# Kernel optimization log

Hardware: AMD Instinct MI355X
Metric: run time of the kernel (lower is better)

## Reference

```python
import jax, jax.numpy as jnp
from jax import lax
import numpy as np

B, L, IN_DIM = 1, 2048, 1024
D_MODEL, D_INNER, D_STATE, DT_RANK, D_CONV, N_LAYERS = 512, 1024, 16, 32, 4, 2


def _ln(x, w, b):
    m = jnp.mean(x, -1, keepdims=True)
    v = jnp.var(x, -1, keepdims=True)
    return (x - m) * lax.rsqrt(v + 1e-5) * w + b


def _rms(x, w):
    return x * lax.rsqrt(jnp.mean(x * x, -1, keepdims=True) + 1e-5) * w


def _assoc_scan(dA, dBx):
    # first-order linear recurrence h_t = dA_t * h_{t-1} + dBx_t via associative scan
    def comb(e1, e2):
        a1, b1 = e1
        a2, b2 = e2
        return a1 * a2, a2 * b1 + b2
    return lax.associative_scan(comb, (dA, dBx), axis=1)[1]


def _mamba_layer(h, in_w, cw, cb, xw, dtw, dtb, alog, Dp, ow, rw):
    hn = _rms(h, rw)                              # pre-norm (RMSNorm)
    xz = hn @ in_w                                # [b,l,2*d_inner]
    xi, z = jnp.split(xz, 2, -1)
    # causal depthwise conv1d (kernel d_conv, left pad d_conv-1)
    xc = lax.conv_general_dilated(xi.transpose(0, 2, 1), cw, (1,), [(D_CONV - 1, 0)],
                                  feature_group_count=D_INNER,
                                  dimension_numbers=('NCH', 'OIH', 'NCH')) + cb[None, :, None]
    xi = jax.nn.silu(xc.transpose(0, 2, 1))       # [b,l,d_inner]
    dbc = xi @ xw                                 # [b,l,dt_rank+2*d_state]
    dt, Bm, Cm = jnp.split(dbc, [DT_RANK, DT_RANK + D_STATE], -1)
    delta = jax.nn.softplus(dt @ dtw + dtb)       # [b,l,d_inner]
    A = -jnp.exp(alog)                            # [d_inner, d_state]
    dA = jnp.exp(delta[..., None] * A)            # [b,l,d_inner,d_state]
    dBx = (delta * xi)[..., None] * Bm[:, :, None, :]
    hs = _assoc_scan(dA, dBx)                     # [b,l,d_inner,d_state]
    y = jnp.einsum('bldn,bln->bld', hs, Cm) + xi * Dp
    y = y * jax.nn.silu(z)
    return h + y @ ow


def _conv_t(x, w, b, s, p):
    # PyTorch ConvTranspose2d, weight layout [Cin, Cout, k, k]
    kT = jnp.flip(w, (2, 3)).transpose(1, 0, 2, 3)
    pad = w.shape[2] - 1 - p
    y = lax.conv_general_dilated(x, kT, (1, 1), [(pad, pad), (pad, pad)],
                                 lhs_dilation=(s, s),
                                 dimension_numbers=('NCHW', 'OIHW', 'NCHW'))
    return y + b[None, :, None, None]


def _fwd(x, coords, W_fc1, b_fc1, W_pos, b_pos,
         mamba_in_w, mamba_conv_w, mamba_conv_b, mamba_x_w, mamba_dt_w, mamba_dt_b,
         mamba_A_log, mamba_D, mamba_out_w, mamba_rms_w,
         ln_w, ln_b, Wa1, ba1, Wa2, ba2,
         ct1_w, ct1_b, ct2_w, ct2_b, ct3_w, ct3_b, ct4_w, ct4_b, ct5_w, ct5_b):
    h = jax.nn.gelu(x @ W_fc1 + b_fc1, approximate=False)   # _fc1
    h = h + (coords @ W_pos + b_pos)[None]                  # linear pos-emb
    for l in range(N_LAYERS):
        h = _mamba_layer(h, mamba_in_w[l], mamba_conv_w[l], mamba_conv_b[l],
                         mamba_x_w[l], mamba_dt_w[l], mamba_dt_b[l],
                         mamba_A_log[l], mamba_D[l], mamba_out_w[l], mamba_rms_w[l])
    h = _ln(h, ln_w, ln_b)
    A = jnp.tanh(h @ Wa1 + ba1) @ Wa2 + ba2                 # [1,L,1]
    A = jax.nn.softmax(A.transpose(0, 2, 1), axis=-1)       # [1,1,L]
    pooled = jnp.einsum('bol,bld->bod', A, h)               # [1,1,512]
    feat = pooled.reshape(x.shape[0], D_MODEL, 1, 1)
    y = jax.nn.relu(_conv_t(feat, ct1_w, ct1_b, 1, 0))      # 1 -> 4
    y = jax.nn.relu(_conv_t(y, ct2_w, ct2_b, 4, 0))         # 4 -> 16
    y = jax.nn.relu(_conv_t(y, ct3_w, ct3_b, 2, 1))         # 16 -> 32
    y = jax.nn.relu(_conv_t(y, ct4_w, ct4_b, 2, 1))         # 32 -> 64
    return _conv_t(y, ct5_w, ct5_b, 2, 1)                   # 64 -> 128, 11 classes


def setup_inputs() -> dict:
    key = jax.random.key(0)
    ks = jax.random.split(key, 32)
    n = lambda k, s, sc=0.02: jax.random.normal(k, s, jnp.float32) * sc
    inp = {
        'x': jax.random.normal(ks[0], (B, L, IN_DIM), jnp.float32),
        'coords': jax.random.uniform(ks[1], (L, 2), jnp.float32),
        'W_fc1': n(ks[2], (IN_DIM, D_MODEL)), 'b_fc1': jnp.zeros((D_MODEL,)),
        'W_pos': n(ks[3], (2, D_MODEL)), 'b_pos': jnp.zeros((D_MODEL,)),
        'mamba_in_w': n(ks[4], (N_LAYERS, D_MODEL, 2 * D_INNER)),
        'mamba_conv_w': n(ks[5], (N_LAYERS, D_INNER, 1, D_CONV), 0.1),
        'mamba_conv_b': jnp.zeros((N_LAYERS, D_INNER)),
        'mamba_x_w': n(ks[6], (N_LAYERS, D_INNER, DT_RANK + 2 * D_STATE)),
        'mamba_dt_w': n(ks[7], (N_LAYERS, DT_RANK, D_INNER), 0.1),
        'mamba_dt_b': jnp.full((N_LAYERS, D_INNER), -4.0, jnp.float32),
        'mamba_A_log': jnp.tile(jnp.log(jnp.arange(1, D_STATE + 1, dtype=jnp.float32)), (N_LAYERS, D_INNER, 1)),
        'mamba_D': jnp.ones((N_LAYERS, D_INNER), jnp.float32),
        'mamba_out_w': n(ks[8], (N_LAYERS, D_INNER, D_MODEL)),
        'mamba_rms_w': jnp.ones((N_LAYERS, D_MODEL), jnp.float32),
        'ln_w': jnp.ones((D_MODEL,)), 'ln_b': jnp.zeros((D_MODEL,)),
        'Wa1': n(ks[9], (D_MODEL, 128)), 'ba1': jnp.zeros((128,)),
        'Wa2': n(ks[10], (128, 1)), 'ba2': jnp.zeros((1,)),
        'ct1_w': n(ks[11], (512, 256, 4, 4)), 'ct1_b': jnp.zeros((256,)),
        'ct2_w': n(ks[12], (256, 128, 4, 4)), 'ct2_b': jnp.zeros((128,)),
        'ct3_w': n(ks[13], (128, 64, 4, 4)), 'ct3_b': jnp.zeros((64,)),
        'ct4_w': n(ks[14], (64, 32, 4, 4)), 'ct4_b': jnp.zeros((32,)),
        'ct5_w': n(ks[15], (32, 11, 4, 4)), 'ct5_b': jnp.zeros((11,)),
    }
    return inp


def reference(x, coords, W_fc1, b_fc1, W_pos, b_pos,
              mamba_in_w, mamba_conv_w, mamba_conv_b, mamba_x_w, mamba_dt_w, mamba_dt_b,
              mamba_A_log, mamba_D, mamba_out_w, mamba_rms_w,
              ln_w, ln_b, Wa1, ba1, Wa2, ba2,
              ct1_w, ct1_b, ct2_w, ct2_b, ct3_w, ct3_b, ct4_w, ct4_b, ct5_w, ct5_b):
    return _fwd(x, coords, W_fc1, b_fc1, W_pos, b_pos,
                mamba_in_w, mamba_conv_w, mamba_conv_b, mamba_x_w, mamba_dt_w, mamba_dt_b,
                mamba_A_log, mamba_D, mamba_out_w, mamba_rms_w,
                ln_w, ln_b, Wa1, ba1, Wa2, ba2,
                ct1_w, ct1_b, ct2_w, ct2_b, ct3_w, ct3_b, ct4_w, ct4_b, ct5_w, ct5_b)
```

## Files before the change

kernel.cpp:

```cpp
#include <hip/hip_runtime.h>
#include <math.h>

#define LSEQ 2048
#define DM 512
#define DI 1024
#define NST 16
#define CHUNK 128
#define NC (LSEQ / CHUNK)

__device__ __forceinline__ float siluf(float v) { return v / (1.f + expf(-v)); }

__global__ __launch_bounds__(128) void gemm_w(
    const float* __restrict__ A, int lda,
    const float* __restrict__ B, int ldb,
    float* __restrict__ out, int ldc, int Ktot)
{
    __shared__ float As[16][192];
    __shared__ float Bs[16][68];
    const int tid = threadIdx.x;
    const int tx = tid & 7, ty = tid >> 3;
    const int n0 = blockIdx.x << 6, m0 = blockIdx.y << 7;
    const int z = blockIdx.z, nz = gridDim.z;
    const int Kz = Ktot / nz, kb = z * Kz;
    const int apos = ((tid >> 3) * 12) + (tid & 7);
    const int bkr = tid >> 3, bcol = (tid & 7) << 3;
    const float* Ap = A + (size_t)(m0 + tid) * lda + kb;
    const float* Bp = B + (size_t)(kb + bkr) * ldb + n0 + bcol;
    float acc[8][8] = {};
    float4 a0 = *(const float4*)(Ap + 0);
    float4 a1 = *(const float4*)(Ap + 4);
    float4 a2 = *(const float4*)(Ap + 8);
    float4 a3 = *(const float4*)(Ap + 12);
    float4 b0 = *(const float4*)(Bp + 0);
    float4 b1 = *(const float4*)(Bp + 4);
    for (int k0 = 0; k0 < Kz; k0 += 16) {
        As[0][apos] = a0.x;  As[1][apos] = a0.y;  As[2][apos] = a0.z;  As[3][apos] = a0.w;
        As[4][apos] = a1.x;  As[5][apos] = a1.y;  As[6][apos] = a1.z;  As[7][apos] = a1.w;
        As[8][apos] = a2.x;  As[9][apos] = a2.y;  As[10][apos] = a2.z; As[11][apos] = a2.w;
        As[12][apos] = a3.x; As[13][apos] = a3.y; As[14][apos] = a3.z; As[15][apos] = a3.w;
        *(float4*)&Bs[bkr][bcol] = b0;
        *(float4*)&Bs[bkr][bcol + 4] = b1;
        __syncthreads();
        if (k0 + 16 < Kz) {
            a0 = *(const float4*)(Ap + k0 + 16);
            a1 = *(const float4*)(Ap + k0 + 20);
            a2 = *(const float4*)(Ap + k0 + 24);
            a3 = *(const float4*)(Ap + k0 + 28);
            b0 = *(const float4*)(Bp + (size_t)(k0 + 16) * ldb);
            b1 = *(const float4*)(Bp + (size_t)(k0 + 16) * ldb + 4);
        }
#pragma unroll
        for (int kk = 0; kk < 16; ++kk) {
            float4 av0 = *(const float4*)&As[kk][ty * 12];
            float4 av1 = *(const float4*)&As[kk][ty * 12 + 4];
            float4 bv0 = *(const float4*)&Bs[kk][tx << 3];
            float4 bv1 = *(const float4*)&Bs[kk][(tx << 3) + 4];
            float a8[8] = {av0.x, av0.y, av0.z, av0.w, av1.x, av1.y, av1.z, av1.w};
            float b8[8] = {bv0.x, bv0.y, bv0.z, bv0.w, bv1.x, bv1.y, bv1.z, bv1.w};
#pragma unroll
            for (int i = 0; i < 8; ++i)
#pragma unroll
                for (int j = 0; j < 8; ++j)
                    acc[i][j] = fmaf(a8[i], b8[j], acc[i][j]);
        }
        __syncthreads();
    }
    const int Mtot = gridDim.y << 7;
    float* op = out + (size_t)z * Mtot * ldc;
#pragma unroll
    for (int i = 0; i < 8; ++i) {
        float* Cp = op + (size_t)(m0 + (ty << 3) + i) * ldc + n0 + (tx << 3);
        *(float4*)Cp = make_float4(acc[i][0], acc[i][1], acc[i][2], acc[i][3]);
        *(float4*)(Cp + 4) = make_float4(acc[i][4], acc[i][5], acc[i][6], acc[i][7]);
    }
}

__global__ __launch_bounds__(256) void sk_reduce(
    const float* part, float* out, int S, int nz, int add)
{
    const int idx = blockIdx.x * 256 + threadIdx.x;
    if (idx >= S) return;
    float s = 0.f;
    for (int zz = 0; zz < nz; ++zz) s += part[(size_t)zz * S + idx];
    if (add) out[idx] += s; else out[idx] = s;
}

__global__ __launch_bounds__(256) void dtproj_k(
    const float* __restrict__ A, const float* __restrict__ B,
    const float* __restrict__ dtb, float* __restrict__ delta)
{
    __shared__ float As[16][68];
    __shared__ float Bs[16][68];
    const int tid = threadIdx.x;
    const int tx = tid & 15, ty = tid >> 4;
    const int m0 = blockIdx.y << 6, n0 = blockIdx.x << 6;
    const int arow = tid >> 2, akk = (tid & 3) << 2;
    const int bkr = tid >> 4, bnn = (tid & 15) << 2;
    const float* Ap = A + (size_t)(m0 + arow) * 64 + akk;
    const float* Bp = B + (size_t)bkr * DI + n0 + bnn;
    float acc[4][4] = {};
    for (int k0 = 0; k0 < 32; k0 += 16) {
        float4 av = *(const float4*)(Ap + k0);
        float4 bv = *(const float4*)(Bp + (size_t)k0 * DI);
        As[akk + 0][arow] = av.x;
        As[akk + 1][arow] = av.y;
        As[akk + 2][arow] = av.z;
        As[akk + 3][arow] = av.w;
        *(float4*)&Bs[bkr][bnn] = bv;
        __syncthreads();
#pragma unroll
        for (int kk = 0; kk < 16; ++kk) {
            float4 a = *(const float4*)&As[kk][ty << 2];
            float4 b = *(const float4*)&Bs[kk][tx << 2];
#pragma unroll
            for (int i = 0; i < 4; ++i) {
                float ai = (i == 0) ? a.x : (i == 1) ? a.y : (i == 2) ? a.z : a.w;
                acc[i][0] = fmaf(ai, b.x, acc[i][0]);
                acc[i][1] = fmaf(ai, b.y, acc[i][1]);
                acc[i][2] = fmaf(ai, b.z, acc[i][2]);
                acc[i][3] = fmaf(ai, b.w, acc[i][3]);
            }
        }
        __syncthreads();
    }
    const int col = n0 + (tx << 2);
    float4 bb = *(const float4*)&dtb[col];
    float bias[4] = {bb.x, bb.y, bb.z, bb.w};
#pragma unroll
    for (int i = 0; i < 4; ++i) {
        float* Cp = delta + (size_t)(m0 + (ty << 2) + i) * DI + col;
#pragma unroll
        for (int j = 0; j < 4; ++j) {
            float v = acc[i][j] + bias[j];
            Cp[j] = fmaxf(v, 0.f) + log1pf(expf(-fabsf(v)));
        }
    }
}

__global__ __launch_bounds__(256) void gemm64(
    const float* __restrict__ A, int lda,
    const float* __restrict__ B, int ldb,
    float* __restrict__ C, int ldc,
    int K, int accum)
{
    __shared__ float As[16][68];
    __shared__ float Bs[16][68];
    const int tid = threadIdx.x;
    const int tx = tid & 15, ty = tid >> 4;
    const int m0 = blockIdx.y << 6, n0 = blockIdx.x << 6;
    const int arow = tid >> 2, akk = (tid & 3) << 2;
    const int bkr = tid >> 4, bnn = (tid & 15) << 2;
    const float* Ap = A + (size_t)(m0 + arow) * lda + akk;
    const float* Bp = B + (size_t)bkr * ldb + n0 + bnn;
    float acc[4][4] = {};
    for (int k0 = 0; k0 < K; k0 += 16) {
        float4 av = *(const float4*)(Ap + k0);
        float4 bv = *(const float4*)(Bp + (size_t)k0 * ldb);
        As[akk + 0][arow] = av.x;
        As[akk + 1][arow] = av.y;
        As[akk + 2][arow] = av.z;
        As[akk + 3][arow] = av.w;
        *(float4*)&Bs[bkr][bnn] = bv;
        __syncthreads();
#pragma unroll
        for (int kk = 0; kk < 16; ++kk) {
            float4 a = *(const float4*)&As[kk][ty << 2];
            float4 b = *(const float4*)&Bs[kk][tx << 2];
            acc[0][0] = fmaf(a.x, b.x, acc[0][0]);
            acc[0][1] = fmaf(a.x, b.y, acc[0][1]);
            acc[0][2] = fmaf(a.x, b.z, acc[0][2]);
            acc[0][3] = fmaf(a.x, b.w, acc[0][3]);
            acc[1][0] = fmaf(a.y, b.x, acc[1][0]);
            acc[1][1] = fmaf(a.y, b.y, acc[1][1]);
            acc[1][2] = fmaf(a.y, b.z, acc[1][2]);
            acc[1][3] = fmaf(a.y, b.w, acc[1][3]);
            acc[2][0] = fmaf(a.z, b.x, acc[2][0]);
            acc[2][1] = fmaf(a.z, b.y, acc[2][1]);
            acc[2][2] = fmaf(a.z, b.z, acc[2][2]);
            acc[2][3] = fmaf(a.z, b.w, acc[2][3]);
            acc[3][0] = fmaf(a.w, b.x, acc[3][0]);
            acc[3][1] = fmaf(a.w, b.y, acc[3][1]);
            acc[3][2] = fmaf(a.w, b.z, acc[3][2]);
            acc[3][3] = fmaf(a.w, b.w, acc[3][3]);
        }
        __syncthreads();
    }
#pragma unroll
    for (int i = 0; i < 4; ++i) {
        float* Cp = C + (size_t)(m0 + (ty << 2) + i) * ldc + n0 + (tx << 2);
        if (accum) {
            Cp[0] += acc[i][0]; Cp[1] += acc[i][1]; Cp[2] += acc[i][2]; Cp[3] += acc[i][3];
        } else {
            Cp[0] = acc[i][0]; Cp[1] = acc[i][1]; Cp[2] = acc[i][2]; Cp[3] = acc[i][3];
        }
    }
}

__global__ __launch_bounds__(256) void xproj_splitk(
    const float* __restrict__ A, const float* __restrict__ B,
    float* __restrict__ part)
{
    __shared__ float As[16][68];
    __shared__ float Bs[16][68];
    const int tid = threadIdx.x;
    const int tx = tid & 15, ty = tid >> 4;
    const int ks = blockIdx.x;
    const int m0 = blockIdx.y << 6;
    const int arow = tid >> 2, ak = (tid & 3) << 2;
    const int bkr = tid >> 4, bcol = (tid & 15) << 2;
    const int kbase = ks << 7;
    const float* Ap = A + (size_t)(m0 + arow) * DI + kbase + ak;
    const float* Bp = B + (size_t)(kbase + bkr) * 64 + bcol;
    float acc[4][4] = {};
    for (int k0 = 0; k0 < 128; k0 += 16) {
        float4 av = *(const float4*)(Ap + k0);
        float4 bv = *(const float4*)(Bp + k0 * 64);
        As[ak + 0][arow] = av.x;
        As[ak + 1][arow] = av.y;
        As[ak + 2][arow] = av.z;
        As[ak + 3][arow] = av.w;
        *(float4*)&Bs[bkr][bcol] = bv;
        __syncthreads();
#pragma unroll
        for (int kk = 0; kk < 16; ++kk) {
            float4 a = *(const float4*)&As[kk][ty << 2];
            float4 b = *(const float4*)&Bs[kk][tx << 2];
            acc[0][0] = fmaf(a.x, b.x, acc[0][0]);
            acc[0][1] = fmaf(a.x, b.y, acc[0][1]);
            acc[0][2] = fmaf(a.x, b.z, acc[0][2]);
            acc[0][3] = fmaf(a.x, b.w, acc[0][3]);
            acc[1][0] = fmaf(a.y, b.x, acc[1][0]);
            acc[1][1] = fmaf(a.y, b.y, acc[1][1]);
            acc[1][2] = fmaf(a.y, b.z, acc[1][2]);
            acc[1][3] = fmaf(a.y, b.w, acc[1][3]);
            acc[2][0] = fmaf(a.z, b.x, acc[2][0]);
            acc[2][1] = fmaf(a.z, b.y, acc[2][1]);
            acc[2][2] = fmaf(a.z, b.z, acc[2][2]);
            acc[2][3] = fmaf(a.z, b.w, acc[2][3]);
            acc[3][0] = fmaf(a.w, b.x, acc[3][0]);
            acc[3][1] = fmaf(a.w, b.y, acc[3][1]);
            acc[3][2] = fmaf(a.w, b.z, acc[3][2]);
            acc[3][3] = fmaf(a.w, b.w, acc[3][3]);
        }
        __syncthreads();
    }
#pragma unroll
    for (int i = 0; i < 4; ++i) {
        float* Cp = part + ((size_t)ks * LSEQ + m0 + (ty << 2) + i) * 64 + (tx << 2);
        Cp[0] = acc[i][0]; Cp[1] = acc[i][1]; Cp[2] = acc[i][2]; Cp[3] = acc[i][3];
    }
}

__global__ __launch_bounds__(256) void xproj_reduce(
    const float* __restrict__ part, float* __restrict__ dbc)
{
    const int idx = blockIdx.x * 256 + threadIdx.x;
    float s = 0.f;
#pragma unroll
    for (int ks = 0; ks < 8; ++ks) s += part[(size_t)ks * LSEQ * 64 + idx];
    dbc[idx] = s;
}

__global__ __launch_bounds__(256) void fc1_fin(
    const float* __restrict__ part,
    const float* __restrict__ bfc1, const float* __restrict__ coords,
    const float* __restrict__ Wpos, const float* __restrict__ bpos,
    const float* __restrict__ rw,
    float* __restrict__ h, float* __restrict__ hn)
{
    const int t = blockIdx.x, tid = threadIdx.x;
    const size_t base = (size_t)t * DM;
    float va = 0.f, vb = 0.f;
#pragma unroll
    for (int z = 0; z < 8; ++z) {
        va += part[(size_t)z * LSEQ * DM + base + tid];
        vb += part[(size_t)z * LSEQ * DM + base + 256 + tid];
    }
    const float cx = coords[2 * t], cy = coords[2 * t + 1];
    va += bfc1[tid];
    vb += bfc1[256 + tid];
    float ga = 0.5f * va * (1.f + erff(va * 0.70710678118654752f));
    float gb = 0.5f * vb * (1.f + erff(vb * 0.70710678118654752f));
    ga += cx * Wpos[tid] + cy * Wpos[DM + tid] + bpos[tid];
    gb += cx * Wpos[256 + tid] + cy * Wpos[DM + 256 + tid] + bpos[256 + tid];
    h[base + tid] = ga;
    h[base + 256 + tid] = gb;
    float ss = ga * ga + gb * gb;
#pragma unroll
    for (int off = 1; off < 64; off <<= 1) ss += __shfl_xor(ss, off);
    __shared__ float red[4];
    if ((tid & 63) == 0) red[tid >> 6] = ss;
    __syncthreads();
    float inv = rsqrtf((red[0] + red[1] + red[2] + red[3]) * (1.f / DM) + 1e-5f);
    hn[base + tid] = ga * inv * rw[tid];
    hn[base + 256 + tid] = gb * inv * rw[256 + tid];
}

__global__ __launch_bounds__(256) void skadd_norm(
    const float* __restrict__ part, float* __restrict__ h,
    const float* __restrict__ w1, const float* __restrict__ b1,
    float* __restrict__ outb, int mode)
{
    const int t = blockIdx.x, tid = threadIdx.x;
    const size_t base = (size_t)t * DM;
    float va = h[base + tid], vb = h[base + 256 + tid];
#pragma unroll
    for (int z = 0; z < 8; ++z) {
        va += part[(size_t)z * LSEQ * DM + base + tid];
        vb += part[(size_t)z * LSEQ * DM + base + 256 + tid];
    }
    h[base + tid] = va;
    h[base + 256 + tid] = vb;
    __shared__ float red1[4], red2[4];
    if (mode == 0) {
        float ss = va * va + vb * vb;
#pragma unroll
        for (int off = 1; off < 64; off <<= 1) ss += __shfl_xor(ss, off);
        if ((tid & 63) == 0) red1[tid >> 6] = ss;
        __syncthreads();
        float inv = rsqrtf((red1[0] + red1[1] + red1[2] + red1[3]) * (1.f / DM) + 1e-5f);
        outb[base + tid] = va * inv * w1[tid];
        outb[base + 256 + tid] = vb * inv * w1[256 + tid];
    } else {
        float s = va + vb;
#pragma unroll
        for (int off = 1; off < 64; off <<= 1) s += __shfl_xor(s, off);
        if ((tid & 63) == 0) red1[tid >> 6] = s;
        __syncthreads();
        float mean = (red1[0] + red1[1] + red1[2] + red1[3]) * (1.f / DM);
        float da = va - mean, db = vb - mean;
        float vs = da * da + db * db;
#pragma unroll
        for (int off = 1; off < 64; off <<= 1) vs += __shfl_xor(vs, off);
        if ((tid & 63) == 0) red2[tid >> 6] = vs;
        __syncthreads();
        float inv = rsqrtf((red2[0] + red2[1] + red2[2] + red2[3]) * (1.f / DM) + 1e-5f);
        outb[base + tid] = da * inv * w1[tid] + b1[tid];
        outb[base + 256 + tid] = db * inv * w1[256 + tid] + b1[256 + tid];
    }
}

__global__ __launch_bounds__(256) void conv_silu_k(
    const float* __restrict__ xz, const float* __restrict__ cw,
    const float* __restrict__ cb, float* __restrict__ xc)
{
    int idx = blockIdx.x * 256 + threadIdx.x;
    int t = idx >> 10, c = idx & 1023;
    float w0 = cw[c * 4], w1 = cw[c * 4 + 1], w2 = cw[c * 4 + 2], w3 = cw[c * 4 + 3];
    float s = cb[c];
    if (t >= 3) s = fmaf(xz[(size_t)(t - 3) * 2048 + c], w0, s);
    if (t >= 2) s = fmaf(xz[(size_t)(t - 2) * 2048 + c], w1, s);
    if (t >= 1) s = fmaf(xz[(size_t)(t - 1) * 2048 + c], w2, s);
    s = fmaf(xz[(size_t)t * 2048 + c], w3, s);
    xc[idx] = siluf(s);
}

__global__ __launch_bounds__(256) void scan_p1(
    const float* __restrict__ delta, const float* __restrict__ xc,
    const float* __restrict__ dbc, const float* __restrict__ alog,
    float* __restrict__ aprod, float* __restrict__ hfin)
{
    __shared__ float sD[CHUNK][16], sX[CHUNK][16], sB[CHUNK][16];
    const int tid = threadIdx.x;
    const int g = tid >> 4, n = tid & 15;
    const int d0 = blockIdx.x << 4;
    const int c = blockIdx.y;
    const int t0 = c * CHUNK;
    const int d = d0 + g;
    const float An = -expf(alog[d * NST + n]);
    for (int i = tid; i < CHUNK * 16; i += 256) {
        int r = i >> 4, cc = i & 15;
        sD[r][cc] = delta[(size_t)(t0 + r) * DI + d0 + cc];
        sX[r][cc] = xc[(size_t)(t0 + r) * DI + d0 + cc];
        sB[r][cc] = dbc[(size_t)(t0 + r) * 64 + 32 + cc];
    }
    __syncthreads();
    float h = 0.f, ap = 1.f;
    for (int i = 0; i < CHUNK; ++i) {
        float dl = sD[i][g], xv = sX[i][g];
        float a = expf(dl * An);
        h = fmaf(a, h, dl * xv * sB[i][n]);
        ap *= a;
    }
    size_t idx = ((size_t)c * DI + d) * NST + n;
    aprod[idx] = ap;
    hfin[idx] = h;
}

__global__ __launch_bounds__(256) void scan_carry(
    const float* __restrict__ aprod, const float* __restrict__ hfin,
    float* __restrict__ carry)
{
    const int dn = blockIdx.x * 256 + threadIdx.x;
    float h = 0.f;
    carry[dn] = 0.f;
#pragma unroll
    for (int c = 0; c < NC - 1; ++c) {
        h = fmaf(aprod[(size_t)c * DI * NST + dn], h, hfin[(size_t)c * DI * NST + dn]);
        carry[(size_t)(c + 1) * DI * NST + dn] = h;
    }
}

__global__ __launch_bounds__(256) void scan_p2(
    const float* __restrict__ delta, const float* __restrict__ xc,
    const float* __restrict__ dbc, const float* __restrict__ xz,
    const float* __restrict__ alog, const float* __restrict__ Dp,
    const float* __restrict__ carry, float* __restrict__ y)
{
    __shared__ float sD[CHUNK][16], sX[CHUNK][16], sB[CHUNK][16], sC[CHUNK][16], sZ[CHUNK][16];
    const int tid = threadIdx.x;
    const int g = tid >> 4, n = tid & 15;
    const int d0 = blockIdx.x << 4;
    const int c = blockIdx.y;
    const int t0 = c * CHUNK;
    const int d = d0 + g;
    const float An = -expf(alog[d * NST + n]);
    const float Dd = Dp[d];
    for (int i = tid; i < CHUNK * 16; i += 256) {
        int r = i >> 4, cc = i & 15;
        sD[r][cc] = delta[(size_t)(t0 + r) * DI + d0 + cc];
        sX[r][cc] = xc[(size_t)(t0 + r) * DI + d0 + cc];
        sB[r][cc] = dbc[(size_t)(t0 + r) * 64 + 32 + cc];
        sC[r][cc] = dbc[(size_t)(t0 + r) * 64 + 48 + cc];
        sZ[r][cc] = xz[(size_t)(t0 + r) * 2048 + 1024 + d0 + cc];
    }
    __syncthreads();
    float h = carry[((size_t)c * DI + d) * NST + n];
    for (int i = 0; i < CHUNK; ++i) {
        float dl = sD[i][g], xv = sX[i][g];
        float a = expf(dl * An);
        h = fmaf(a, h, dl * xv * sB[i][n]);
        float p = h * sC[i][n];
        p += __shfl_xor(p, 1, 16);
        p += __shfl_xor(p, 2, 16);
        p += __shfl_xor(p, 4, 16);
        p += __shfl_xor(p, 8, 16);
        if (n == 0) {
            float yv = p + xv * Dd;
            float zz = sZ[i][g];
            y[(size_t)(t0 + i) * DI + d] = yv * siluf(zz);
        }
    }
}

__global__ __launch_bounds__(256) void attn_fin(
    const float* __restrict__ amx, const float* __restrict__ ba1,
    const float* __restrict__ Wa2, const float* __restrict__ ba2,
    float* __restrict__ scores)
{
    const int tid = threadIdx.x;
    const int row = blockIdx.x * 4 + (tid >> 6);
    const int lane = tid & 63;
    float v = tanhf(amx[(size_t)row * 128 + lane] + ba1[lane]) * Wa2[lane]
            + tanhf(amx[(size_t)row * 128 + 64 + lane] + ba1[64 + lane]) * Wa2[64 + lane];
#pragma unroll
    for (int off = 1; off < 64; off <<= 1) v += __shfl_xor(v, off);
    if (lane == 0) scores[row] = v + ba2[0];
}

__global__ __launch_bounds__(1024) void softmax_k(
    const float* __restrict__ s, float* __restrict__ w)
{
    const int tid = threadIdx.x;
    __shared__ float red[16];
    float m = fmaxf(s[tid], s[tid + 1024]);
#pragma unroll
    for (int off = 1; off < 64; off <<= 1) m = fmaxf(m, __shfl_xor(m, off));
    if ((tid & 63) == 0) red[tid >> 6] = m;
    __syncthreads();
    if (tid < 64) {
        float mm = (tid < 16) ? red[tid] : -1e30f;
#pragma unroll
        for (int off = 1; off < 16; off <<= 1) mm = fmaxf(mm, __shfl_xor(mm, off));
        if (tid == 0) red[0] = mm;
    }
    __syncthreads();
    const float gm = red[0];
    __syncthreads();
    float e0 = expf(s[tid] - gm), e1 = expf(s[tid + 1024] - gm);
    float sum = e0 + e1;
#pragma unroll
    for (int off = 1; off < 64; off <<= 1) sum += __shfl_xor(sum, off);
    __shared__ float red2[16];
    if ((tid & 63) == 0) red2[tid >> 6] = sum;
    __syncthreads();
    if (tid < 64) {
        float ss = (tid < 16) ? red2[tid] : 0.f;
#pragma unroll
        for (int off = 1; off < 16; off <<= 1) ss += __shfl_xor(ss, off);
        if (tid == 0) red2[0] = ss;
    }
    __syncthreads();
    float inv = 1.f / red2[0];
    w[tid] = e0 * inv;
    w[tid + 1024] = e1 * inv;
}

__global__ __launch_bounds__(256) void pooled_p1(
    const float* __restrict__ wts, const float* __restrict__ hf, float* __restrict__ part)
{
    const int j = blockIdx.x * 256 + threadIdx.x;
    const int tc = blockIdx.y;
    float acc = 0.f;
    const int t0 = tc * 128;
    for (int t = t0; t < t0 + 128; ++t) acc = fmaf(wts[t], hf[(size_t)t * DM + j], acc);
    part[(size_t)tc * DM + j] = acc;
}

__global__ __launch_bounds__(256) void pooled_p2(
    const float* __restrict__ part, float* __restrict__ pooled)
{
    const int j = blockIdx.x * 256 + threadIdx.x;
    float acc = 0.f;
#pragma unroll
    for (int tc = 0; tc < 16; ++tc) acc += part[(size_t)tc * DM + j];
    pooled[j] = acc;
}

__global__ __launch_bounds__(256) void ct1_fast(
    const float* __restrict__ feat, const float* __restrict__ w,
    const float* __restrict__ b, float* __restrict__ out)
{
    __shared__ float sf[512];
    __shared__ float sRed[256];
    const int o = blockIdx.x, tid = threadIdx.x;
    sf[tid] = feat[tid];
    sf[tid + 256] = feat[tid + 256];
    __syncthreads();
    const int p = tid & 15, g = tid >> 4;
    float acc = 0.f;
#pragma unroll 8
    for (int ci = g * 32; ci < g * 32 + 32; ++ci)
        acc = fmaf(sf[ci], w[ci * 4096 + (o << 4) + p], acc);
    sRed[tid] = acc;
    __syncthreads();
    if (g == 0) {
        float s = b[o];
#pragma unroll
        for (int gg = 0; gg < 16; ++gg) s += sRed[gg * 16 + p];
        out[(o << 4) + p] = fmaxf(s, 0.f);
    }
}

__global__ __launch_bounds__(256) void ct2_fast(
    const float* __restrict__ in, const float* __restrict__ w,
    const float* __restrict__ b, float* __restrict__ out)
{
    __shared__ float sI[1024];
    __shared__ float sW[1024];
    __shared__ float sRed[256];
    const int yy = blockIdx.x, o = blockIdx.y, tid = threadIdx.x;
    const int iy = yy >> 2, ky = yy & 3;
    for (int i = tid; i < 1024; i += 256) {
        int ci = i >> 2, q = i & 3;
        sI[i] = in[(ci << 4) + (iy << 2) + q];
        sW[i] = w[ci * 2048 + (o << 4) + (ky << 2) + q];
    }
    __syncthreads();
    const int xx = tid & 15, g = tid >> 4;
    const int ix = xx >> 2, kx = xx & 3;
    float acc = 0.f;
#pragma unroll 8
    for (int ci = g * 16; ci < g * 16 + 16; ++ci)
        acc = fmaf(sI[(ci << 2) + ix], sW[(ci << 2) + kx], acc);
    sRed[tid] = acc;
    __syncthreads();
    if (g == 0) {
        float s = b[o];
#pragma unroll
        for (int gg = 0; gg < 16; ++gg) s += sRed[gg * 16 + xx];
        out[(o << 8) + (yy << 4) + xx] = fmaxf(s, 0.f);
    }
}

__global__ __launch_bounds__(256) void ctup_fast(
    const float* __restrict__ in, const float* __restrict__ w,
    const float* __restrict__ b, float* __restrict__ out,
    int Cin, int Cout, int Hin, int hshift, int relu)
{
    __shared__ float sIn[4608];
    __shared__ float sW[2048];
    __shared__ float sRed[256];
    const int tid = threadIdx.x;
    const int yy = blockIdx.x, o = blockIdx.y;
    const int Hout = Hin << 1;
    const int ST = Hin + 2;
    const int houtshift = hshift + 1;

    const int ky0 = (yy + 1) & 1;
    const int iy0 = (yy + 1 - ky0) >> 1;
    const int iy1 = iy0 - 1;
    const int row_elems = Cin * ST;

    for (int i = tid; i < 2 * row_elems; i += 256) sIn[i] = 0.f;
    __syncthreads();
    const int nload = Cin << hshift;
    if (iy0 < Hin) {
        const float* src = in + ((size_t)iy0 << hshift);
        for (int i = tid; i < nload; i += 256) {
            int ci = i >> hshift, col = i & (Hin - 1);
            sIn[ci * ST + 1 + col] = src[((size_t)ci << (2 * hshift)) + col];
        }
    }
    if (iy1 >= 0) {
        const float* src = in + ((size_t)iy1 << hshift);
        for (int i = tid; i < nload; i += 256) {
            int ci = i >> hshift, col = i & (Hin - 1);
            sIn[row_elems + ci * ST + 1 + col] = src[((size_t)ci << (2 * hshift)) + col];
        }
    }
    for (int i = tid; i < (Cin << 4); i += 256)
        sW[i] = w[(size_t)(i >> 4) * (Cout << 4) + (o << 4) + (i & 15)];
    __syncthreads();

    const int xx = tid & (Hout - 1);
    const int g = tid >> houtshift;
    const int kx0 = (xx + 1) & 1;
    const int ix0 = (xx + 1 - kx0) >> 1;
    const int k00 = (ky0 << 2) + kx0;

    float acc = 0.f;
    const float* in1 = sIn + row_elems;
#pragma unroll 4
    for (int ci = g * 16; ci < g * 16 + 16; ++ci) {
        const int base = ci * ST + ix0;
        const float* wr = &sW[ci << 4];
        float i00 = sIn[base + 1], i01 = sIn[base];
        float i10 = in1[base + 1], i11 = in1[base];
        acc = fmaf(i00, wr[k00], acc);
        acc = fmaf(i01, wr[k00 + 2], acc);
        acc = fmaf(i10, wr[k00 + 8], acc);
        acc = fmaf(i11, wr[k00 + 10], acc);
    }
    sRed[tid] = acc;
    __syncthreads();
    if (g == 0) {
        float s = b[o];
        const int XG = 256 >> houtshift;
        for (int gg = 0; gg < XG; ++gg) s += sRed[(gg << houtshift) + xx];
        out[(size_t)o * Hout * Hout + (size_t)yy * Hout + xx] = relu ? fmaxf(s, 0.f) : s;
    }
}

extern "C" void kernel_launch(void* const* d_in, const int* in_sizes, int n_in,
                              void* d_out, int out_size, void* d_ws, size_t ws_size,
                              hipStream_t stream)
{
    const float* x      = (const float*)d_in[0];
    const float* coords = (const float*)d_in[1];
    const float* Wfc1   = (const float*)d_in[2];
    const float* bfc1   = (const float*)d_in[3];
    const float* Wpos   = (const float*)d_in[4];
    const float* bpos   = (const float*)d_in[5];
    const float* in_w   = (const float*)d_in[6];
    const float* conv_w = (const float*)d_in[7];
    const float* conv_b = (const float*)d_in[8];
    const float* x_w    = (const float*)d_in[9];
    const float* dt_w   = (const float*)d_in[10];
    const float* dt_b   = (const float*)d_in[11];
    const float* A_log  = (const float*)d_in[12];
    const float* Dp     = (const float*)d_in[13];
    const float* out_w  = (const float*)d_in[14];
    const float* rms_w  = (const float*)d_in[15];
    const float* ln_w   = (const float*)d_in[16];
    const float* ln_b   = (const float*)d_in[17];
    const float* Wa1    = (const float*)d_in[18];
    const float* ba1    = (const float*)d_in[19];
    const float* Wa2    = (const float*)d_in[20];
    const float* ba2    = (const float*)d_in[21];
    const float* ct1w   = (const float*)d_in[22];
    const float* ct1b   = (const float*)d_in[23];
    const float* ct2w   = (const float*)d_in[24];
    const float* ct2b   = (const float*)d_in[25];
    const float* ct3w   = (const float*)d_in[26];
    const float* ct3b   = (const float*)d_in[27];
    const float* ct4w   = (const float*)d_in[28];
    const float* ct4b   = (const float*)d_in[29];
    const float* ct5w   = (const float*)d_in[30];
    const float* ct5b   = (const float*)d_in[31];

    float* ws     = (float*)d_ws;
    float* h      = ws;
    float* hn     = h + (size_t)LSEQ * DM;
    float* xz     = hn + (size_t)LSEQ * DM;
    float* xc     = xz + (size_t)LSEQ * 2 * DI;
    float* dbc    = xc + (size_t)LSEQ * DI;
    float* delta  = dbc + (size_t)LSEQ * 64;
    float* yb     = delta + (size_t)LSEQ * DI;
    float* hf     = yb + (size_t)LSEQ * DI;
    float* scores = hf + (size_t)LSEQ * DM;
    float* wts    = scores + LSEQ;
    float* pooled = wts + LSEQ;
    float* c1     = pooled + DM;
    float* c2     = c1 + 256 * 16;
    float* c3     = c2 + 128 * 256;
    float* c4     = c3 + 64 * 1024;
    float* aprod  = c4 + 32 * 4096;
    float* hfin   = aprod + (size_t)NC * DI * NST;
    float* carry  = hfin + (size_t)NC * DI * NST;
    float* part   = carry + (size_t)NC * DI * NST;
    float* partk  = yb;
    float* skpart = xz;
    float* amx    = xz;

    gemm_w<<<dim3(DM / 64, LSEQ / 128, 8), 128, 0, stream>>>(x, 1024, Wfc1, DM, skpart, DM, 1024);
    fc1_fin<<<LSEQ, 256, 0, stream>>>(skpart, bfc1, coords, Wpos, bpos, rms_w, h, hn);

    for (int l = 0; l < 2; ++l) {
        gemm_w<<<dim3(2 * DI / 64, LSEQ / 128, 2), 128, 0, stream>>>(
            hn, DM, in_w + (size_t)l * DM * 2 * DI, 2 * DI, xz, 2 * DI, 512);
        sk_reduce<<<LSEQ * 2 * DI / 256, 256, 0, stream>>>(xz, xz, LSEQ * 2 * DI, 2, 0);
        conv_silu_k<<<LSEQ * DI / 256, 256, 0, stream>>>(
            xz, conv_w + (size_t)l * DI * 4, conv_b + (size_t)l * DI, xc);
        xproj_splitk<<<dim3(8, LSEQ / 64), 256, 0, stream>>>(
            xc, x_w + (size_t)l * DI * 64, partk);
        xproj_reduce<<<LSEQ * 64 / 256, 256, 0, stream>>>(partk, dbc);
        dtproj_k<<<dim3(DI / 64, LSEQ / 64), 256, 0, stream>>>(
            dbc, dt_w + (size_t)l * 32 * DI, dt_b + (size_t)l * DI, delta);
        scan_p1<<<dim3(DI / 16, NC), 256, 0, stream>>>(
            delta, xc, dbc, A_log + (size_t)l * DI * NST, aprod, hfin);
        scan_carry<<<DI * NST / 256, 256, 0, stream>>>(aprod, hfin, carry);
        scan_p2<<<dim3(DI / 16, NC), 256, 0, stream>>>(
            delta, xc, dbc, xz, A_log + (size_t)l * DI * NST, Dp + (size_t)l * DI,
            carry, yb);
        gemm_w<<<dim3(DM / 64, LSEQ / 128, 8), 128, 0, stream>>>(
            yb, DI, out_w + (size_t)l * DI * DM, DM, skpart, DM, 1024);
        if (l == 0)
            skadd_norm<<<LSEQ, 256, 0, stream>>>(skpart, h, rms_w + DM, nullptr, hn, 0);
        else
            skadd_norm<<<LSEQ, 256, 0, stream>>>(skpart, h, ln_w, ln_b, hf, 1);
    }

    gemm64<<<dim3(2, LSEQ / 64), 256, 0, stream>>>(hf, DM, Wa1, 128, amx, 128, DM, 0);
    attn_fin<<<LSEQ / 4, 256, 0, stream>>>(amx, ba1, Wa2, ba2, scores);
    softmax_k<<<1, 1024, 0, stream>>>(scores, wts);
    pooled_p1<<<dim3(2, 16), 256, 0, stream>>>(wts, hf, part);
    pooled_p2<<<2, 256, 0, stream>>>(part, pooled);

    ct1_fast<<<256, 256, 0, stream>>>(pooled, ct1w, ct1b, c1);
    ct2_fast<<<dim3(16, 128), 256, 0, stream>>>(c1, ct2w, ct2b, c2);
    ctup_fast<<<dim3(32, 64), 256, 0, stream>>>(c2, ct3w, ct3b, c3, 128, 64, 16, 4, 1);
    ctup_fast<<<dim3(64, 32), 256, 0, stream>>>(c3, ct4w, ct4b, c4, 64, 32, 32, 5, 1);
    ctup_fast<<<dim3(128, 11), 256, 0, stream>>>(c4, ct5w, ct5b, (float*)d_out, 32, 11, 64, 6, 0);
}
```

Measured before the change: 705.6 us.

## Restructure selective scan to per-channel threads and replace split-K in_proj GEMM

The chunked scan kernels now assign one thread per d_inner channel holding all 16 state values in registers. Each thread reads delta/x/z directly with a one-step prefetch, and the 16-way shuffle reduction for y is replaced by a register dot product. Chunk size drops from 128 to 64 and the aprod/hfin/carry buffers are transposed to [chunk][n][d] for coalesced access. The in_proj GEMM switches from a 2-way split-K plus a separate reduce kernel to a single 64x64-tile GEMM without split-K, removing a full pass over the xz buffer. The cost is higher register pressure per thread and fewer scan blocks (8x32 blocks of 128 threads), which may limit occupancy on the scan.

```diff
diff --git a/kernel.cpp b/kernel.cpp
--- a/kernel.cpp
+++ b/kernel.cpp
@@ -5,10 +5,70 @@
 #define DM 512
 #define DI 1024
 #define NST 16
-#define CHUNK 128
+#define CHUNK 64
 #define NC (LSEQ / CHUNK)
 
 __device__ __forceinline__ float siluf(float v) { return v / (1.f + expf(-v)); }
+
+__global__ __launch_bounds__(128) void gemm_s(
+    const float* __restrict__ A, int lda,
+    const float* __restrict__ B, int ldb,
+    float* __restrict__ out, int ldc, int Ktot)
+{
+    __shared__ float As[16][68];
+    __shared__ float Bs[16][68];
+    const int tid = threadIdx.x;
+    const int tx = tid & 7, ty = tid >> 3;
+    const int n0 = blockIdx.x << 6, m0 = blockIdx.y << 6;
+    const int z = blockIdx.z, nz = gridDim.z;
+    const int Kz = Ktot / nz, kb = z * Kz;
+    const int arow = tid >> 1, ak = (tid & 1) << 3;
+    const int bkr = tid >> 3, bcol = (tid & 7) << 3;
+    const float* Ap = A + (size_t)(m0 + arow) * lda + kb + ak;
+    const float* Bp = B + (size_t)(kb + bkr) * ldb + n0 + bcol;
+    float acc[4][8] = {};
+    float4 a0 = *(const float4*)(Ap);
+    float4 a1 = *(const float4*)(Ap + 4);
+    float4 b0 = *(const float4*)(Bp);
+    float4 b1 = *(const float4*)(Bp + 4);
+    for (int k0 = 0; k0 < Kz; k0 += 16) {
+        As[ak + 0][arow] = a0.x; As[ak + 1][arow] = a0.y;
+        As[ak + 2][arow] = a0.z; As[ak + 3][arow] = a0.w;
+        As[ak + 4][arow] = a1.x; As[ak + 5][arow] = a1.y;
+        As[ak + 6][arow] = a1.z; As[ak + 7][arow] = a1.w;
+        *(float4*)&Bs[bkr][bcol] = b0;
+        *(float4*)&Bs[bkr][bcol + 4] = b1;
+        __syncthreads();
+        if (k0 + 16 < Kz) {
+            a0 = *(const float4*)(Ap + k0 + 16);
+            a1 = *(const float4*)(Ap + k0 + 20);
+            b0 = *(const float4*)(Bp + (size_t)(k0 + 16) * ldb);
+            b1 = *(const float4*)(Bp + (size_t)(k0 + 16) * ldb + 4);
+        }
+#pragma unroll
+        for (int kk = 0; kk < 16; ++kk) {
+            float4 a = *(const float4*)&As[kk][ty << 2];
+            float4 bb0 = *(const float4*)&Bs[kk][tx << 3];
+            float4 bb1 = *(const float4*)&Bs[kk][(tx << 3) + 4];
+            float av[4] = {a.x, a.y, a.z, a.w};
+            float bv[8] = {bb0.x, bb0.y, bb0.z, bb0.w, bb1.x, bb1.y, bb1.z, bb1.w};
+#pragma unroll
+            for (int i = 0; i < 4; ++i)
+#pragma unroll
+                for (int j = 0; j < 8; ++j)
+                    acc[i][j] = fmaf(av[i], bv[j], acc[i][j]);
+        }
+        __syncthreads();
+    }
+    const int Mtot = gridDim.y << 6;
+    float* op = out + (size_t)z * Mtot * ldc;
+#pragma unroll
+    for (int i = 0; i < 4; ++i) {
+        float* Cp = op + (size_t)(m0 + (ty << 2) + i) * ldc + n0 + (tx << 3);
+        *(float4*)Cp = make_float4(acc[i][0], acc[i][1], acc[i][2], acc[i][3]);
+        *(float4*)(Cp + 4) = make_float4(acc[i][4], acc[i][5], acc[i][6], acc[i][7]);
+    }
+}
 
 __global__ __launch_bounds__(128) void gemm_w(
     const float* __restrict__ A, int lda,
@@ -75,16 +135,6 @@
     }
 }
 
-__global__ __launch_bounds__(256) void sk_reduce(
-    const float* part, float* out, int S, int nz, int add)
-{
-    const int idx = blockIdx.x * 256 + threadIdx.x;
-    if (idx >= S) return;
-    float s = 0.f;
-    for (int zz = 0; zz < nz; ++zz) s += part[(size_t)zz * S + idx];
-    if (add) out[idx] += s; else out[idx] = s;
-}
-
 __global__ __launch_bounds__(256) void dtproj_k(
     const float* __restrict__ A, const float* __restrict__ B,
     const float* __restrict__ dtb, float* __restrict__ delta)
@@ -355,91 +405,124 @@
     xc[idx] = siluf(s);
 }
 
-__global__ __launch_bounds__(256) void scan_p1(
+__global__ __launch_bounds__(128) void scan_p1(
     const float* __restrict__ delta, const float* __restrict__ xc,
     const float* __restrict__ dbc, const float* __restrict__ alog,
     float* __restrict__ aprod, float* __restrict__ hfin)
 {
-    __shared__ float sD[CHUNK][16], sX[CHUNK][16], sB[CHUNK][16];
-    const int tid = threadIdx.x;
-    const int g = tid >> 4, n = tid & 15;
-    const int d0 = blockIdx.x << 4;
+    __shared__ float sB[CHUNK][16];
+    const int tid = threadIdx.x;
+    const int d = (blockIdx.x << 7) + tid;
     const int c = blockIdx.y;
     const int t0 = c * CHUNK;
-    const int d = d0 + g;
-    const float An = -expf(alog[d * NST + n]);
-    for (int i = tid; i < CHUNK * 16; i += 256) {
-        int r = i >> 4, cc = i & 15;
-        sD[r][cc] = delta[(size_t)(t0 + r) * DI + d0 + cc];
-        sX[r][cc] = xc[(size_t)(t0 + r) * DI + d0 + cc];
-        sB[r][cc] = dbc[(size_t)(t0 + r) * 64 + 32 + cc];
-    }
-    __syncthreads();
-    float h = 0.f, ap = 1.f;
+    for (int i = tid; i < CHUNK * 16; i += 128)
+        sB[i >> 4][i & 15] = dbc[(size_t)(t0 + (i >> 4)) * 64 + 32 + (i & 15)];
+    float An[NST];
+#pragma unroll
+    for (int n = 0; n < NST; ++n) An[n] = -expf(alog[d * NST + n]);
+    __syncthreads();
+    float h[NST] = {}, ap[NST];
+#pragma unroll
+    for (int n = 0; n < NST; ++n) ap[n] = 1.f;
+    float dl = delta[(size_t)t0 * DI + d];
+    float xv = xc[(size_t)t0 * DI + d];
     for (int i = 0; i < CHUNK; ++i) {
-        float dl = sD[i][g], xv = sX[i][g];
-        float a = expf(dl * An);
-        h = fmaf(a, h, dl * xv * sB[i][n]);
-        ap *= a;
-    }
-    size_t idx = ((size_t)c * DI + d) * NST + n;
-    aprod[idx] = ap;
-    hfin[idx] = h;
+        float dln = 0.f, xvn = 0.f;
+        if (i + 1 < CHUNK) {
+            dln = delta[(size_t)(t0 + i + 1) * DI + d];
+            xvn = xc[(size_t)(t0 + i + 1) * DI + d];
+        }
+        const float dlx = dl * xv;
+        float4 b0 = *(const float4*)&sB[i][0];
+        float4 b1 = *(const float4*)&sB[i][4];
+        float4 b2 = *(const float4*)&sB[i][8];
+        float4 b3 = *(const float4*)&sB[i][12];
+        float Bv[NST] = {b0.x, b0.y, b0.z, b0.w, b1.x, b1.y, b1.z, b1.w,
+                         b2.x, b2.y, b2.z, b2.w, b3.x, b3.y, b3.z, b3.w};
+#pragma unroll
+        for (int n = 0; n < NST; ++n) {
+            float a = expf(dl * An[n]);
+            h[n] = fmaf(a, h[n], dlx * Bv[n]);
+            ap[n] *= a;
+        }
+        dl = dln; xv = xvn;
+    }
+#pragma unroll
+    for (int n = 0; n < NST; ++n) {
+        aprod[((size_t)c * NST + n) * DI + d] = ap[n];
+        hfin[((size_t)c * NST + n) * DI + d] = h[n];
+    }
 }
 
 __global__ __launch_bounds__(256) void scan_carry(
     const float* __restrict__ aprod, const float* __restrict__ hfin,
     float* __restrict__ carry)
 {
-    const int dn = blockIdx.x * 256 + threadIdx.x;
+    const int idx = blockIdx.x * 256 + threadIdx.x;
     float h = 0.f;
-    carry[dn] = 0.f;
-#pragma unroll
+    carry[idx] = 0.f;
     for (int c = 0; c < NC - 1; ++c) {
-        h = fmaf(aprod[(size_t)c * DI * NST + dn], h, hfin[(size_t)c * DI * NST + dn]);
-        carry[(size_t)(c + 1) * DI * NST + dn] = h;
-    }
-}
-
-__global__ __launch_bounds__(256) void scan_p2(
+        h = fmaf(aprod[(size_t)c * NST * DI + idx], h, hfin[(size_t)c * NST * DI + idx]);
+        carry[(size_t)(c + 1) * NST * DI + idx] = h;
+    }
+}
+
+__global__ __launch_bounds__(128) void scan_p2(
     const float* __restrict__ delta, const float* __restrict__ xc,
     const float* __restrict__ dbc, const float* __restrict__ xz,
     const float* __restrict__ alog, const float* __restrict__ Dp,
     const float* __restrict__ carry, float* __restrict__ y)
 {
-    __shared__ float sD[CHUNK][16], sX[CHUNK][16], sB[CHUNK][16], sC[CHUNK][16], sZ[CHUNK][16];
-    const int tid = threadIdx.x;
-    const int g = tid >> 4, n = tid & 15;
-    const int d0 = blockIdx.x << 4;
+    __shared__ float sB[CHUNK][16];
+    __shared__ float sC[CHUNK][16];
+    const int tid = threadIdx.x;
+    const int d = (blockIdx.x << 7) + tid;
     const int c = blockIdx.y;
     const int t0 = c * CHUNK;
-    const int d = d0 + g;
-    const float An = -expf(alog[d * NST + n]);
+    for (int i = tid; i < CHUNK * 16; i += 128) {
+        sB[i >> 4][i & 15] = dbc[(size_t)(t0 + (i >> 4)) * 64 + 32 + (i & 15)];
+        sC[i >> 4][i & 15] = dbc[(size_t)(t0 + (i >> 4)) * 64 + 48 + (i & 15)];
+    }
+    float An[NST];
+#pragma unroll
+    for (int n = 0; n < NST; ++n) An[n] = -expf(alog[d * NST + n]);
     const float Dd = Dp[d];
-    for (int i = tid; i < CHUNK * 16; i += 256) {
-        int r = i >> 4, cc = i & 15;
-        sD[r][cc] = delta[(size_t)(t0 + r) * DI + d0 + cc];
-        sX[r][cc] = xc[(size_t)(t0 + r) * DI + d0 + cc];
-        sB[r][cc] = dbc[(size_t)(t0 + r) * 64 + 32 + cc];
-        sC[r][cc] = dbc[(size_t)(t0 + r) * 64 + 48 + cc];
-        sZ[r][cc] = xz[(size_t)(t0 + r) * 2048 + 1024 + d0 + cc];
-    }
-    __syncthreads();
-    float h = carry[((size_t)c * DI + d) * NST + n];
+    float h[NST];
+#pragma unroll
+    for (int n = 0; n < NST; ++n) h[n] = carry[((size_t)c * NST + n) * DI + d];
+    __syncthreads();
+    float dl = delta[(size_t)t0 * DI + d];
+    float xv = xc[(size_t)t0 * DI + d];
+    float zz = xz[(size_t)t0 * 2048 + 1024 + d];
     for (int i = 0; i < CHUNK; ++i) {
-        float dl = sD[i][g], xv = sX[i][g];
-        float a = expf(dl * An);
-        h = fmaf(a, h, dl * xv * sB[i][n]);
-        float p = h * sC[i][n];
-        p += __shfl_xor(p, 1, 16);
-        p += __shfl_xor(p, 2, 16);
-        p += __shfl_xor(p, 4, 16);
-        p += __shfl_xor(p, 8, 16);
-        if (n == 0) {
-            float yv = p + xv * Dd;
-            float zz = sZ[i][g];
-            y[(size_t)(t0 + i) * DI + d] = yv * siluf(zz);
-        }
+        float dln = 0.f, xvn = 0.f, zzn = 0.f;
+        if (i + 1 < CHUNK) {
+            dln = delta[(size_t)(t0 + i + 1) * DI + d];
+            xvn = xc[(size_t)(t0 + i + 1) * DI + d];
+            zzn = xz[(size_t)(t0 + i + 1) * 2048 + 1024 + d];
+        }
+        const float dlx = dl * xv;
+        float4 b0 = *(const float4*)&sB[i][0];
+        float4 b1 = *(const float4*)&sB[i][4];
+        float4 b2 = *(const float4*)&sB[i][8];
+        float4 b3 = *(const float4*)&sB[i][12];
+        float4 c0 = *(const float4*)&sC[i][0];
+        float4 c1 = *(const float4*)&sC[i][4];
+        float4 c2 = *(const float4*)&sC[i][8];
+        float4 c3 = *(const float4*)&sC[i][12];
+        float Bv[NST] = {b0.x, b0.y, b0.z, b0.w, b1.x, b1.y, b1.z, b1.w,
+                         b2.x, b2.y, b2.z, b2.w, b3.x, b3.y, b3.z, b3.w};
+        float Cv[NST] = {c0.x, c0.y, c0.z, c0.w, c1.x, c1.y, c1.z, c1.w,
+                         c2.x, c2.y, c2.z, c2.w, c3.x, c3.y, c3.z, c3.w};
+        float p = 0.f;
+#pragma unroll
+        for (int n = 0; n < NST; ++n) {
+            float a = expf(dl * An[n]);
+            h[n] = fmaf(a, h[n], dlx * Bv[n]);
+            p = fmaf(h[n], Cv[n], p);
+        }
+        y[(size_t)(t0 + i) * DI + d] = (p + xv * Dd) * siluf(zz);
+        dl = dln; xv = xvn; zz = zzn;
     }
 }
 
@@ -696,9 +779,9 @@
     float* c3     = c2 + 128 * 256;
     float* c4     = c3 + 64 * 1024;
     float* aprod  = c4 + 32 * 4096;
-    float* hfin   = aprod + (size_t)NC * DI * NST;
-    float* carry  = hfin + (size_t)NC * DI * NST;
-    float* part   = carry + (size_t)NC * DI * NST;
+    float* hfin   = aprod + (size_t)NC * NST * DI;
+    float* carry  = hfin + (size_t)NC * NST * DI;
+    float* part   = carry + (size_t)NC * NST * DI;
     float* partk  = yb;
     float* skpart = xz;
     float* amx    = xz;
@@ -707,9 +790,8 @@
     fc1_fin<<<LSEQ, 256, 0, stream>>>(skpart, bfc1, coords, Wpos, bpos, rms_w, h, hn);
 
     for (int l = 0; l < 2; ++l) {
-        gemm_w<<<dim3(2 * DI / 64, LSEQ / 128, 2), 128, 0, stream>>>(
-            hn, DM, in_w + (size_t)l * DM * 2 * DI, 2 * DI, xz, 2 * DI, 512);
-        sk_reduce<<<LSEQ * 2 * DI / 256, 256, 0, stream>>>(xz, xz, LSEQ * 2 * DI, 2, 0);
+        gemm_s<<<dim3(2 * DI / 64, LSEQ / 64, 1), 128, 0, stream>>>(
+            hn, DM, in_w + (size_t)l * DM * 2 * DI, 2 * DI, xz, 2 * DI, DM);
         conv_silu_k<<<LSEQ * DI / 256, 256, 0, stream>>>(
             xz, conv_w + (size_t)l * DI * 4, conv_b + (size_t)l * DI, xc);
         xproj_splitk<<<dim3(8, LSEQ / 64), 256, 0, stream>>>(
@@ -717,10 +799,10 @@
         xproj_reduce<<<LSEQ * 64 / 256, 256, 0, stream>>>(partk, dbc);
         dtproj_k<<<dim3(DI / 64, LSEQ / 64), 256, 0, stream>>>(
             dbc, dt_w + (size_t)l * 32 * DI, dt_b + (size_t)l * DI, delta);
-        scan_p1<<<dim3(DI / 16, NC), 256, 0, stream>>>(
+        scan_p1<<<dim3(DI / 128, NC), 128, 0, stream>>>(
             delta, xc, dbc, A_log + (size_t)l * DI * NST, aprod, hfin);
-        scan_carry<<<DI * NST / 256, 256, 0, stream>>>(aprod, hfin, carry);
-        scan_p2<<<dim3(DI / 16, NC), 256, 0, stream>>>(
+        scan_carry<<<NST * DI / 256, 256, 0, stream>>>(aprod, hfin, carry);
+        scan_p2<<<dim3(DI / 128, NC), 128, 0, stream>>>(
             delta, xc, dbc, xz, A_log + (size_t)l * DI * NST, Dp + (size_t)l * DI,
             carry, yb);
         gemm_w<<<dim3(DM / 64, LSEQ / 128, 8), 128, 0, stream>>>(
```

After: 727.8 us. 3.1% more time.
